# Kernel tuning notes

Hardware: AMD Instinct MI355X
Metric: run time of the kernel (lower is better)

## Reference

```python
import jax, jax.numpy as jnp
import numpy as np

N, HW, L = 16, 3136, 64
C_IN, C_OUT, D = 256, 512, 256


def setup_inputs() -> dict:
    key = jax.random.key(0)
    ks = jax.random.split(key, 8)
    # xavier-normal-ish scale for weights
    def xav(k, shape):
        fan_in, fan_out = shape[1], shape[0]
        std = (2.0 / (fan_in + fan_out)) ** 0.5
        return jax.random.normal(k, shape, dtype=jnp.float32) * std
    return {
        "x": jax.random.normal(ks[0], (N, HW, C_IN), dtype=jnp.float32),
        "t": jax.random.normal(ks[1], (N, L, D), dtype=jnp.float32),
        "W1": xav(ks[2], (D, C_IN)),      # linear1 weight (out,in), no bias
        "W2": xav(ks[3], (D, D)),         # linear2 weight, no bias
        "W3": xav(ks[4], (C_OUT, D)),     # linear3 weight
        "b3": jnp.zeros((C_OUT,), dtype=jnp.float32),
        "Wd": xav(ks[5], (C_OUT, C_IN)),  # downsample weight
        "bd": jnp.zeros((C_OUT,), dtype=jnp.float32),
    }


def reference(x, t, W1, W2, W3, b3, Wd, bd):
    # x: (N, HW, C_in), t: (N, L, D)
    x_q = jnp.einsum("npc,dc->npd", x, W1)          # (N, HW, D)
    t_q = jnp.einsum("nld,ed->nle", t, W2)          # (N, L, D)
    a = jnp.einsum("npd,nld->npl", x_q, t_q)        # unscaled QK^T (N, HW, L)
    a = jax.nn.softmax(a, axis=2)
    t3 = jnp.einsum("nld,od->nlo", t, W3) + b3      # (N, L, C_out)
    av = jnp.einsum("npl,nlo->npo", a, t3)          # (N, HW, C_out)
    x_ds = jnp.einsum("npc,oc->npo", x, Wd) + bd    # downsample residual
    return x_ds + av
```

## Files before the change

kernel.cpp:

```cpp
#include <hip/hip_runtime.h>


typedef unsigned short u16;
using half8 = __attribute__((ext_vector_type(8))) _Float16;
using f32x4 = __attribute__((ext_vector_type(4))) float;

__device__ __forceinline__ u16 f2h(float f) {
  _Float16 h = (_Float16)f;
  union { _Float16 h; u16 u; } cv; cv.h = h;
  return cv.u;
}

__device__ __forceinline__ f32x4 mfma16(half8 a, half8 b, f32x4 c) {
  return __builtin_amdgcn_mfma_f32_16x16x32_f16(a, b, c, 0, 0, 0);
}

__global__ __launch_bounds__(256) void cvt_kernel(
    const float* __restrict__ W1, const float* __restrict__ W2,
    const float* __restrict__ W3, const float* __restrict__ Wd,
    const float* __restrict__ t,
    u16* __restrict__ W1h, u16* __restrict__ W2h, u16* __restrict__ W3h,
    u16* __restrict__ Wdh, u16* __restrict__ th) {
  int i = blockIdx.x * 256 + threadIdx.x;
  if (i < 65536)  { W1h[i] = f2h(W1[i]); W2h[i] = f2h(W2[i]); }
  if (i < 131072) { W3h[i] = f2h(W3[i]); Wdh[i] = f2h(Wd[i]); }
  if (i < 262144) { th[i]  = f2h(t[i]); }
}

__global__ __launch_bounds__(256) void tq_kernel(
    const u16* __restrict__ th, const u16* __restrict__ W2h,
    u16* __restrict__ tqh) {
  const int n = blockIdx.x >> 2, eb = blockIdx.x & 3;
  const int tid = threadIdx.x, w = tid >> 6, lane = tid & 63;
  const int quad = lane >> 4, l16 = lane & 15;
  const int e0 = eb*64 + w*16;

  f32x4 acc[4];
  #pragma unroll
  for (int mt = 0; mt < 4; ++mt) acc[mt] = (f32x4){0.f, 0.f, 0.f, 0.f};

  #pragma unroll
  for (int k = 0; k < 8; ++k) {
    half8 b = *(const half8*)(W2h + (size_t)(e0 + l16)*256 + k*32 + quad*8);
    #pragma unroll
    for (int mt = 0; mt < 4; ++mt) {
      half8 a = *(const half8*)(th + (size_t)(n*64 + mt*16 + l16)*256 + k*32 + quad*8);
      acc[mt] = mfma16(a, b, acc[mt]);
    }
  }
  #pragma unroll
  for (int mt = 0; mt < 4; ++mt)
    #pragma unroll
    for (int r = 0; r < 4; ++r) {
      int l = mt*16 + quad*4 + r;
      tqh[(size_t)(n*64 + l)*256 + e0 + l16] = f2h(acc[mt][r]);
    }
}

__global__ __launch_bounds__(256) void t3t_kernel(
    const u16* __restrict__ th, const u16* __restrict__ W3h,
    const float* __restrict__ b3, u16* __restrict__ t3Th) {
  const int n = blockIdx.x >> 3, ob = blockIdx.x & 7;
  const int tid = threadIdx.x, w = tid >> 6, lane = tid & 63;
  const int quad = lane >> 4, l16 = lane & 15;
  const int o0 = ob*64 + w*16;

  f32x4 acc[4];
  #pragma unroll
  for (int nt = 0; nt < 4; ++nt) acc[nt] = (f32x4){0.f, 0.f, 0.f, 0.f};

  #pragma unroll
  for (int k = 0; k < 8; ++k) {
    half8 a = *(const half8*)(W3h + (size_t)(o0 + l16)*256 + k*32 + quad*8);
    #pragma unroll
    for (int nt = 0; nt < 4; ++nt) {
      half8 b = *(const half8*)(th + (size_t)(n*64 + nt*16 + l16)*256 + k*32 + quad*8);
      acc[nt] = mfma16(a, b, acc[nt]);
    }
  }
  #pragma unroll
  for (int nt = 0; nt < 4; ++nt)
    #pragma unroll
    for (int r = 0; r < 4; ++r) {
      int o = o0 + quad*4 + r;
      int l = nt*16 + l16;
      t3Th[(size_t)(n*512 + o)*64 + l] = f2h(acc[nt][r] + b3[o]);
    }
}

__global__ __launch_bounds__(512, 4) void main_kernel(
    const float* __restrict__ x, const u16* __restrict__ W1h,
    const u16* __restrict__ Wdh, const u16* __restrict__ tqh,
    const u16* __restrict__ t3Th, const float* __restrict__ bd,
    float* __restrict__ out) {
  __shared__ u16 xs[64*264];
  __shared__ u16 xqaw[64*136];

  const int bid = blockIdx.x;
  const int n = bid / 49;
  const int pt = bid - n*49;
  const int m0 = pt * 64;
  const int tid = threadIdx.x, w = tid >> 6, lane = tid & 63;
  const int quad = lane >> 4, l16 = lane & 15;

  {
    const float4* xg = (const float4*)(x + (size_t)(n*3136 + m0)*256);
    #pragma unroll
    for (int it = 0; it < 8; ++it) {
      int idx = it*512 + tid;
      int r = idx >> 6, c4 = idx & 63;
      float4 v = xg[idx];
      ushort4 u;
      u.x = f2h(v.x); u.y = f2h(v.y); u.z = f2h(v.z); u.w = f2h(v.w);
      *(ushort4*)(&xs[r*264 + c4*4]) = u;
    }
  }
  __syncthreads();

  f32x4 acc2[4];
  #pragma unroll
  for (int lt = 0; lt < 4; ++lt) acc2[lt] = (f32x4){0.f, 0.f, 0.f, 0.f};

  #pragma unroll
  for (int h = 0; h < 2; ++h) {
    f32x4 acc1[4];
    #pragma unroll
    for (int mt = 0; mt < 4; ++mt) acc1[mt] = (f32x4){0.f, 0.f, 0.f, 0.f};

    #pragma unroll
    for (int k = 0; k < 8; ++k) {
      half8 b = *(const half8*)(W1h + (size_t)(h*128 + w*16 + l16)*256 + k*32 + quad*8);
      #pragma unroll
      for (int mt = 0; mt < 4; ++mt) {
        half8 a = *(const half8*)(&xs[(mt*16 + l16)*264 + k*32 + quad*8]);
        acc1[mt] = mfma16(a, b, acc1[mt]);
      }
    }
    __syncthreads();
    #pragma unroll
    for (int mt = 0; mt < 4; ++mt)
      #pragma unroll
      for (int r = 0; r < 4; ++r)
        xqaw[(mt*16 + quad*4 + r)*136 + w*16 + l16] = f2h(acc1[mt][r]);
    __syncthreads();

    if (w < 4) {
      #pragma unroll
      for (int k2 = 0; k2 < 4; ++k2) {
        half8 a = *(const half8*)(&xqaw[(w*16 + l16)*136 + k2*32 + quad*8]);
        #pragma unroll
        for (int lt = 0; lt < 4; ++lt) {
          half8 b = *(const half8*)(tqh + (size_t)(n*64 + lt*16 + l16)*256 + h*128 + k2*32 + quad*8);
          acc2[lt] = mfma16(a, b, acc2[lt]);
        }
      }
    }
  }
  __syncthreads();

  if (w < 4) {
    #pragma unroll
    for (int r = 0; r < 4; ++r) {
      float s0 = acc2[0][r], s1 = acc2[1][r], s2 = acc2[2][r], s3 = acc2[3][r];
      float mx = fmaxf(fmaxf(s0, s1), fmaxf(s2, s3));
      #pragma unroll
      for (int off = 8; off >= 1; off >>= 1) mx = fmaxf(mx, __shfl_xor(mx, off, 64));
      float e0 = __expf(s0 - mx), e1 = __expf(s1 - mx);
      float e2 = __expf(s2 - mx), e3 = __expf(s3 - mx);
      float s = e0 + e1 + e2 + e3;
      #pragma unroll
      for (int off = 8; off >= 1; off >>= 1) s += __shfl_xor(s, off, 64);
      float inv = 1.0f / s;
      int row = (w*16 + quad*4 + r)*72;
      xqaw[row +  0 + l16] = f2h(e0 * inv);
      xqaw[row + 16 + l16] = f2h(e1 * inv);
      xqaw[row + 32 + l16] = f2h(e2 * inv);
      xqaw[row + 48 + l16] = f2h(e3 * inv);
    }
  }
  __syncthreads();

  f32x4 acc[4][4];
  #pragma unroll
  for (int mt = 0; mt < 4; ++mt)
    #pragma unroll
    for (int ot = 0; ot < 4; ++ot) acc[mt][ot] = (f32x4){0.f, 0.f, 0.f, 0.f};

  #pragma unroll
  for (int k3 = 0; k3 < 2; ++k3) {
    half8 a[4];
    #pragma unroll
    for (int mt = 0; mt < 4; ++mt)
      a[mt] = *(const half8*)(&xqaw[(mt*16 + l16)*72 + k3*32 + quad*8]);
    #pragma unroll
    for (int ot = 0; ot < 4; ++ot) {
      half8 b = *(const half8*)(t3Th + (size_t)(n*512 + w*64 + ot*16 + l16)*64 + k3*32 + quad*8);
      #pragma unroll
      for (int mt = 0; mt < 4; ++mt) acc[mt][ot] = mfma16(a[mt], b, acc[mt][ot]);
    }
  }
  #pragma unroll
  for (int k = 0; k < 8; ++k) {
    half8 a[4];
    #pragma unroll
    for (int mt = 0; mt < 4; ++mt)
      a[mt] = *(const half8*)(&xs[(mt*16 + l16)*264 + k*32 + quad*8]);
    #pragma unroll
    for (int ot = 0; ot < 4; ++ot) {
      half8 b = *(const half8*)(Wdh + (size_t)(w*64 + ot*16 + l16)*256 + k*32 + quad*8);
      #pragma unroll
      for (int mt = 0; mt < 4; ++mt) acc[mt][ot] = mfma16(a[mt], b, acc[mt][ot]);
    }
  }

  #pragma unroll
  for (int ot = 0; ot < 4; ++ot) {
    int o = w*64 + ot*16 + l16;
    float bias = bd[o];
    #pragma unroll
    for (int mt = 0; mt < 4; ++mt)
      #pragma unroll
      for (int r = 0; r < 4; ++r) {
        int m = m0 + mt*16 + quad*4 + r;
        out[(size_t)(n*3136 + m)*512 + o] = acc[mt][ot][r] + bias;
      }
  }
}

extern "C" void kernel_launch(void* const* d_in, const int* in_sizes, int n_in,
                              void* d_out, int out_size, void* d_ws, size_t ws_size,
                              hipStream_t stream) {
  const float* x  = (const float*)d_in[0];
  const float* t  = (const float*)d_in[1];
  const float* W1 = (const float*)d_in[2];
  const float* W2 = (const float*)d_in[3];
  const float* W3 = (const float*)d_in[4];
  const float* b3 = (const float*)d_in[5];
  const float* Wd = (const float*)d_in[6];
  const float* bd = (const float*)d_in[7];
  float* out = (float*)d_out;

  char* ws = (char*)d_ws;
  u16* W1h  = (u16*)(ws + 0);
  u16* W2h  = (u16*)(ws + 131072);
  u16* W3h  = (u16*)(ws + 262144);
  u16* Wdh  = (u16*)(ws + 524288);
  u16* th   = (u16*)(ws + 786432);
  u16* tqh  = (u16*)(ws + 1310720);
  u16* t3Th = (u16*)(ws + 1835008);

  hipLaunchKernelGGL(cvt_kernel, dim3(1024), dim3(256), 0, stream,
                     W1, W2, W3, Wd, t, W1h, W2h, W3h, Wdh, th);
  hipLaunchKernelGGL(tq_kernel, dim3(64), dim3(256), 0, stream, th, W2h, tqh);
  hipLaunchKernelGGL(t3t_kernel, dim3(128), dim3(256), 0, stream, th, W3h, b3, t3Th);
  hipLaunchKernelGGL(main_kernel, dim3(784), dim3(512), 0, stream,
                     x, W1h, Wdh, tqh, t3Th, bd, out);
}
```

Measured before the change: 238.6 us.

## Pre-swizzle fp16 operands into MFMA fragment layout and stage output stores via LDS

Operand matrices (weights, t, tq, t3) are written by the conversion and precompute kernels in a fragment-blocked layout, so each lane's half8 load in the MFMA loops is a contiguous 1KB-per-wave read instead of strided row gathers. The tq and t3 kernels are merged into one launch to cut launch overhead. The main kernel now routes accumulators through shared memory in 8-row chunks and writes the output as coalesced float4 rows instead of scattered 4-byte stores, with the bias loaded up front. This adds extra __syncthreads and LDS traffic in the epilogue in exchange for better global store coalescing.

```diff
diff --git a/kernel.cpp b/kernel.cpp
--- a/kernel.cpp
+++ b/kernel.cpp
@@ -15,86 +15,90 @@
   return __builtin_amdgcn_mfma_f32_16x16x32_f16(a, b, c, 0, 0, 0);
 }
 
-__global__ __launch_bounds__(256) void cvt_kernel(
+__global__ __launch_bounds__(256) void reblock_kernel(
     const float* __restrict__ W1, const float* __restrict__ W2,
     const float* __restrict__ W3, const float* __restrict__ Wd,
     const float* __restrict__ t,
-    u16* __restrict__ W1h, u16* __restrict__ W2h, u16* __restrict__ W3h,
-    u16* __restrict__ Wdh, u16* __restrict__ th) {
-  int i = blockIdx.x * 256 + threadIdx.x;
-  if (i < 65536)  { W1h[i] = f2h(W1[i]); W2h[i] = f2h(W2[i]); }
-  if (i < 131072) { W3h[i] = f2h(W3[i]); Wdh[i] = f2h(Wd[i]); }
-  if (i < 262144) { th[i]  = f2h(t[i]); }
-}
-
-__global__ __launch_bounds__(256) void tq_kernel(
-    const u16* __restrict__ th, const u16* __restrict__ W2h,
-    u16* __restrict__ tqh) {
-  const int n = blockIdx.x >> 2, eb = blockIdx.x & 3;
+    u16* __restrict__ W1f, u16* __restrict__ W2f, u16* __restrict__ W3f,
+    u16* __restrict__ Wdf, u16* __restrict__ tf) {
+  int b = blockIdx.x, k = threadIdx.x;
+  const float* src; u16* dst; int row;
+  if (b < 256)       { src = W1; dst = W1f; row = b; }
+  else if (b < 512)  { src = W2; dst = W2f; row = b - 256; }
+  else if (b < 1024) { src = W3; dst = W3f; row = b - 512; }
+  else if (b < 1536) { src = Wd; dst = Wdf; row = b - 1024; }
+  else               { src = t;  dst = tf;  row = b - 1536; }
+  float v = src[(size_t)row*256 + k];
+  int flat = ((row >> 4)*8 + (k >> 5))*512 + ((k >> 3) & 3)*128 + (row & 15)*8 + (k & 7);
+  dst[flat] = f2h(v);
+}
+
+__global__ __launch_bounds__(256) void tq_t3t_kernel(
+    const u16* __restrict__ tf, const u16* __restrict__ W2f,
+    const u16* __restrict__ W3f, const float* __restrict__ b3,
+    u16* __restrict__ tqf, u16* __restrict__ t3f) {
   const int tid = threadIdx.x, w = tid >> 6, lane = tid & 63;
   const int quad = lane >> 4, l16 = lane & 15;
-  const int e0 = eb*64 + w*16;
-
-  f32x4 acc[4];
-  #pragma unroll
-  for (int mt = 0; mt < 4; ++mt) acc[mt] = (f32x4){0.f, 0.f, 0.f, 0.f};
-
-  #pragma unroll
-  for (int k = 0; k < 8; ++k) {
-    half8 b = *(const half8*)(W2h + (size_t)(e0 + l16)*256 + k*32 + quad*8);
-    #pragma unroll
-    for (int mt = 0; mt < 4; ++mt) {
-      half8 a = *(const half8*)(th + (size_t)(n*64 + mt*16 + l16)*256 + k*32 + quad*8);
-      acc[mt] = mfma16(a, b, acc[mt]);
-    }
-  }
-  #pragma unroll
-  for (int mt = 0; mt < 4; ++mt)
-    #pragma unroll
-    for (int r = 0; r < 4; ++r) {
-      int l = mt*16 + quad*4 + r;
-      tqh[(size_t)(n*64 + l)*256 + e0 + l16] = f2h(acc[mt][r]);
-    }
-}
-
-__global__ __launch_bounds__(256) void t3t_kernel(
-    const u16* __restrict__ th, const u16* __restrict__ W3h,
-    const float* __restrict__ b3, u16* __restrict__ t3Th) {
-  const int n = blockIdx.x >> 3, ob = blockIdx.x & 7;
-  const int tid = threadIdx.x, w = tid >> 6, lane = tid & 63;
-  const int quad = lane >> 4, l16 = lane & 15;
-  const int o0 = ob*64 + w*16;
-
-  f32x4 acc[4];
-  #pragma unroll
-  for (int nt = 0; nt < 4; ++nt) acc[nt] = (f32x4){0.f, 0.f, 0.f, 0.f};
-
-  #pragma unroll
-  for (int k = 0; k < 8; ++k) {
-    half8 a = *(const half8*)(W3h + (size_t)(o0 + l16)*256 + k*32 + quad*8);
-    #pragma unroll
-    for (int nt = 0; nt < 4; ++nt) {
-      half8 b = *(const half8*)(th + (size_t)(n*64 + nt*16 + l16)*256 + k*32 + quad*8);
-      acc[nt] = mfma16(a, b, acc[nt]);
-    }
-  }
-  #pragma unroll
-  for (int nt = 0; nt < 4; ++nt)
-    #pragma unroll
-    for (int r = 0; r < 4; ++r) {
-      int o = o0 + quad*4 + r;
-      int l = nt*16 + l16;
-      t3Th[(size_t)(n*512 + o)*64 + l] = f2h(acc[nt][r] + b3[o]);
-    }
+  const int b = blockIdx.x;
+
+  if (b < 64) {
+    const int n = b >> 2, eb = b & 3;
+    const int gW2 = eb*4 + w;
+    f32x4 acc[4];
+    #pragma unroll
+    for (int mt = 0; mt < 4; ++mt) acc[mt] = (f32x4){0.f, 0.f, 0.f, 0.f};
+    #pragma unroll
+    for (int kc = 0; kc < 8; ++kc) {
+      half8 bf = *(const half8*)(W2f + (gW2*8 + kc)*512 + lane*8);
+      #pragma unroll
+      for (int mt = 0; mt < 4; ++mt) {
+        half8 a = *(const half8*)(tf + ((n*4 + mt)*8 + kc)*512 + lane*8);
+        acc[mt] = mfma16(a, bf, acc[mt]);
+      }
+    }
+    #pragma unroll
+    for (int mt = 0; mt < 4; ++mt)
+      #pragma unroll
+      for (int r = 0; r < 4; ++r) {
+        int flat = ((n*4 + mt)*8 + eb*2 + (w >> 1))*512
+                 + ((w & 1)*2 + (l16 >> 3))*128 + (quad*4 + r)*8 + (l16 & 7);
+        tqf[flat] = f2h(acc[mt][r]);
+      }
+  } else {
+    const int b2 = b - 64;
+    const int n = b2 >> 3, ob = b2 & 7;
+    const int gW3 = ob*4 + w;
+    f32x4 acc[4];
+    #pragma unroll
+    for (int nt = 0; nt < 4; ++nt) acc[nt] = (f32x4){0.f, 0.f, 0.f, 0.f};
+    #pragma unroll
+    for (int kc = 0; kc < 8; ++kc) {
+      half8 a = *(const half8*)(W3f + (gW3*8 + kc)*512 + lane*8);
+      #pragma unroll
+      for (int nt = 0; nt < 4; ++nt) {
+        half8 bf = *(const half8*)(tf + ((n*4 + nt)*8 + kc)*512 + lane*8);
+        acc[nt] = mfma16(a, bf, acc[nt]);
+      }
+    }
+    #pragma unroll
+    for (int nt = 0; nt < 4; ++nt)
+      #pragma unroll
+      for (int r = 0; r < 4; ++r) {
+        int o = ob*64 + w*16 + quad*4 + r;
+        int flat = ((n*32 + ob*4 + w)*2 + (nt >> 1))*512
+                 + ((nt & 1)*2 + (l16 >> 3))*128 + (quad*4 + r)*8 + (l16 & 7);
+        t3f[flat] = f2h(acc[nt][r] + b3[o]);
+      }
+  }
 }
 
 __global__ __launch_bounds__(512, 4) void main_kernel(
-    const float* __restrict__ x, const u16* __restrict__ W1h,
-    const u16* __restrict__ Wdh, const u16* __restrict__ tqh,
-    const u16* __restrict__ t3Th, const float* __restrict__ bd,
+    const float* __restrict__ x, const u16* __restrict__ W1f,
+    const u16* __restrict__ Wdf, const u16* __restrict__ tqf,
+    const u16* __restrict__ t3f, const float* __restrict__ bd,
     float* __restrict__ out) {
   __shared__ u16 xs[64*264];
-  __shared__ u16 xqaw[64*136];
+  __shared__ __align__(16) u16 pool[64*136];
 
   const int bid = blockIdx.x;
   const int n = bid / 49;
@@ -102,6 +106,10 @@
   const int m0 = pt * 64;
   const int tid = threadIdx.x, w = tid >> 6, lane = tid & 63;
   const int quad = lane >> 4, l16 = lane & 15;
+
+  float bias[4];
+  #pragma unroll
+  for (int ot = 0; ot < 4; ++ot) bias[ot] = bd[w*64 + ot*16 + l16];
 
   {
     const float4* xg = (const float4*)(x + (size_t)(n*3136 + m0)*256);
@@ -127,13 +135,14 @@
     #pragma unroll
     for (int mt = 0; mt < 4; ++mt) acc1[mt] = (f32x4){0.f, 0.f, 0.f, 0.f};
 
-    #pragma unroll
-    for (int k = 0; k < 8; ++k) {
-      half8 b = *(const half8*)(W1h + (size_t)(h*128 + w*16 + l16)*256 + k*32 + quad*8);
+    const u16* w1p = W1f + (h*8 + w)*8*512;
+    #pragma unroll
+    for (int kc = 0; kc < 8; ++kc) {
+      half8 bf = *(const half8*)(w1p + kc*512 + lane*8);
       #pragma unroll
       for (int mt = 0; mt < 4; ++mt) {
-        half8 a = *(const half8*)(&xs[(mt*16 + l16)*264 + k*32 + quad*8]);
-        acc1[mt] = mfma16(a, b, acc1[mt]);
+        half8 a = *(const half8*)(&xs[(mt*16 + l16)*264 + kc*32 + quad*8]);
+        acc1[mt] = mfma16(a, bf, acc1[mt]);
       }
     }
     __syncthreads();
@@ -141,17 +150,17 @@
     for (int mt = 0; mt < 4; ++mt)
       #pragma unroll
       for (int r = 0; r < 4; ++r)
-        xqaw[(mt*16 + quad*4 + r)*136 + w*16 + l16] = f2h(acc1[mt][r]);
+        pool[(mt*16 + quad*4 + r)*136 + w*16 + l16] = f2h(acc1[mt][r]);
     __syncthreads();
 
     if (w < 4) {
       #pragma unroll
       for (int k2 = 0; k2 < 4; ++k2) {
-        half8 a = *(const half8*)(&xqaw[(w*16 + l16)*136 + k2*32 + quad*8]);
+        half8 a = *(const half8*)(&pool[(w*16 + l16)*136 + k2*32 + quad*8]);
         #pragma unroll
         for (int lt = 0; lt < 4; ++lt) {
-          half8 b = *(const half8*)(tqh + (size_t)(n*64 + lt*16 + l16)*256 + h*128 + k2*32 + quad*8);
-          acc2[lt] = mfma16(a, b, acc2[lt]);
+          half8 bf = *(const half8*)(tqf + ((n*4 + lt)*8 + h*4 + k2)*512 + lane*8);
+          acc2[lt] = mfma16(a, bf, acc2[lt]);
         }
       }
     }
@@ -172,10 +181,10 @@
       for (int off = 8; off >= 1; off >>= 1) s += __shfl_xor(s, off, 64);
       float inv = 1.0f / s;
       int row = (w*16 + quad*4 + r)*72;
-      xqaw[row +  0 + l16] = f2h(e0 * inv);
-      xqaw[row + 16 + l16] = f2h(e1 * inv);
-      xqaw[row + 32 + l16] = f2h(e2 * inv);
-      xqaw[row + 48 + l16] = f2h(e3 * inv);
+      pool[row +  0 + l16] = f2h(e0 * inv);
+      pool[row + 16 + l16] = f2h(e1 * inv);
+      pool[row + 32 + l16] = f2h(e2 * inv);
+      pool[row + 48 + l16] = f2h(e3 * inv);
     }
   }
   __syncthreads();
@@ -187,43 +196,54 @@
     for (int ot = 0; ot < 4; ++ot) acc[mt][ot] = (f32x4){0.f, 0.f, 0.f, 0.f};
 
   #pragma unroll
-  for (int k3 = 0; k3 < 2; ++k3) {
+  for (int kc3 = 0; kc3 < 2; ++kc3) {
     half8 a[4];
     #pragma unroll
     for (int mt = 0; mt < 4; ++mt)
-      a[mt] = *(const half8*)(&xqaw[(mt*16 + l16)*72 + k3*32 + quad*8]);
+      a[mt] = *(const half8*)(&pool[(mt*16 + l16)*72 + kc3*32 + quad*8]);
     #pragma unroll
     for (int ot = 0; ot < 4; ++ot) {
-      half8 b = *(const half8*)(t3Th + (size_t)(n*512 + w*64 + ot*16 + l16)*64 + k3*32 + quad*8);
-      #pragma unroll
-      for (int mt = 0; mt < 4; ++mt) acc[mt][ot] = mfma16(a[mt], b, acc[mt][ot]);
-    }
-  }
-  #pragma unroll
-  for (int k = 0; k < 8; ++k) {
+      half8 bf = *(const half8*)(t3f + ((n*32 + w*4 + ot)*2 + kc3)*512 + lane*8);
+      #pragma unroll
+      for (int mt = 0; mt < 4; ++mt) acc[mt][ot] = mfma16(a[mt], bf, acc[mt][ot]);
+    }
+  }
+  #pragma unroll
+  for (int kc = 0; kc < 8; ++kc) {
     half8 a[4];
     #pragma unroll
     for (int mt = 0; mt < 4; ++mt)
-      a[mt] = *(const half8*)(&xs[(mt*16 + l16)*264 + k*32 + quad*8]);
+      a[mt] = *(const half8*)(&xs[(mt*16 + l16)*264 + kc*32 + quad*8]);
     #pragma unroll
     for (int ot = 0; ot < 4; ++ot) {
-      half8 b = *(const half8*)(Wdh + (size_t)(w*64 + ot*16 + l16)*256 + k*32 + quad*8);
-      #pragma unroll
-      for (int mt = 0; mt < 4; ++mt) acc[mt][ot] = mfma16(a[mt], b, acc[mt][ot]);
-    }
-  }
-
-  #pragma unroll
-  for (int ot = 0; ot < 4; ++ot) {
-    int o = w*64 + ot*16 + l16;
-    float bias = bd[o];
-    #pragma unroll
-    for (int mt = 0; mt < 4; ++mt)
-      #pragma unroll
-      for (int r = 0; r < 4; ++r) {
-        int m = m0 + mt*16 + quad*4 + r;
-        out[(size_t)(n*3136 + m)*512 + o] = acc[mt][ot][r] + bias;
-      }
+      half8 bf = *(const half8*)(Wdf + ((w*4 + ot)*8 + kc)*512 + lane*8);
+      #pragma unroll
+      for (int mt = 0; mt < 4; ++mt) acc[mt][ot] = mfma16(a[mt], bf, acc[mt][ot]);
+    }
+  }
+  __syncthreads();
+
+  float* pf = (float*)pool;
+  #pragma unroll
+  for (int c = 0; c < 8; ++c) {
+    int mt = c >> 1;
+    if ((quad >> 1) == (c & 1)) {
+      int rl = (quad & 1)*4;
+      #pragma unroll
+      for (int ot = 0; ot < 4; ++ot)
+        #pragma unroll
+        for (int r = 0; r < 4; ++r)
+          pf[(rl + r)*520 + w*64 + ot*16 + l16] = acc[mt][ot][r] + bias[ot];
+    }
+    __syncthreads();
+    #pragma unroll
+    for (int j = 0; j < 2; ++j) {
+      int flat = j*512 + tid;
+      int rl = flat >> 7, c4 = (flat & 127)*4;
+      float4 v = *(float4*)&pf[rl*520 + c4];
+      *(float4*)&out[(size_t)(n*3136 + m0 + c*8 + rl)*512 + c4] = v;
+    }
+    __syncthreads();
   }
 }
 
@@ -241,18 +261,18 @@
   float* out = (float*)d_out;
 
   char* ws = (char*)d_ws;
-  u16* W1h  = (u16*)(ws + 0);
-  u16* W2h  = (u16*)(ws + 131072);
-  u16* W3h  = (u16*)(ws + 262144);
-  u16* Wdh  = (u16*)(ws + 524288);
-  u16* th   = (u16*)(ws + 786432);
-  u16* tqh  = (u16*)(ws + 1310720);
-  u16* t3Th = (u16*)(ws + 1835008);
-
-  hipLaunchKernelGGL(cvt_kernel, dim3(1024), dim3(256), 0, stream,
-                     W1, W2, W3, Wd, t, W1h, W2h, W3h, Wdh, th);
-  hipLaunchKernelGGL(tq_kernel, dim3(64), dim3(256), 0, stream, th, W2h, tqh);
-  hipLaunchKernelGGL(t3t_kernel, dim3(128), dim3(256), 0, stream, th, W3h, b3, t3Th);
+  u16* W1f = (u16*)(ws + 0);
+  u16* W2f = (u16*)(ws + 131072);
+  u16* W3f = (u16*)(ws + 262144);
+  u16* Wdf = (u16*)(ws + 524288);
+  u16* tf  = (u16*)(ws + 786432);
+  u16* tqf = (u16*)(ws + 1310720);
+  u16* t3f = (u16*)(ws + 1835008);
+
+  hipLaunchKernelGGL(reblock_kernel, dim3(2560), dim3(256), 0, stream,
+                     W1, W2, W3, Wd, t, W1f, W2f, W3f, Wdf, tf);
+  hipLaunchKernelGGL(tq_t3t_kernel, dim3(192), dim3(256), 0, stream,
+                     tf, W2f, W3f, b3, tqf, t3f);
   hipLaunchKernelGGL(main_kernel, dim3(784), dim3(512), 0, stream,
-                     x, W1h, Wdh, tqh, t3Th, bd, out);
-}
+                     x, W1f, Wdf, tqf, t3f, bd, out);
+}
```

New measurement: 200.4 us. 16.0% less time.
